# Performance work log

Hardware: AMD Instinct MI355X
Metric: run time of the kernel (lower is better)

The kernel has to match this reference:

```python
import jax, jax.numpy as jnp
import numpy as np

NUM_GROUPS = 32
EPS = 1e-6


def group_norm(x, scale, bias):
    # x: [B, C, H, W]
    b, c, h, w = x.shape
    g = NUM_GROUPS
    xg = x.reshape(b, g, c // g, h, w)
    mean = xg.mean(axis=(2, 3, 4), keepdims=True)
    var = xg.var(axis=(2, 3, 4), keepdims=True)
    xg = (xg - mean) * jax.lax.rsqrt(var + EPS)
    x = xg.reshape(b, c, h, w)
    return x * scale[None, :, None, None] + bias[None, :, None, None]


def conv1x1(x, w, b):
    # x: [B, C, H, W], w: [O, C] (1x1 conv weight), b: [O]
    return jnp.einsum('oc,bchw->bohw', w, x) + b[None, :, None, None]


def setup_inputs() -> dict:
    key = jax.random.key(0)
    ks = jax.random.split(key, 6)
    B, C, H, W = 8, 512, 64, 64
    s = 1.0 / np.sqrt(C)
    return {
        'x': jax.random.normal(ks[0], (B, C, H, W), dtype=jnp.float32),
        'gn_scale': jnp.ones((C,), jnp.float32),
        'gn_bias': jnp.zeros((C,), jnp.float32),
        'wq': jax.random.normal(ks[1], (C, C), jnp.float32) * s,
        'bq': jnp.zeros((C,), jnp.float32),
        'wk': jax.random.normal(ks[2], (C, C), jnp.float32) * s,
        'bk': jnp.zeros((C,), jnp.float32),
        'wv': jax.random.normal(ks[3], (C, C), jnp.float32) * s,
        'bv': jnp.zeros((C,), jnp.float32),
        'wo': jax.random.normal(ks[4], (C, C), jnp.float32) * s,
        'bo': jnp.zeros((C,), jnp.float32),
    }


def reference(x, gn_scale, gn_bias, wq, bq, wk, bk, wv, bv, wo, bo):
    b, c, h, w = x.shape
    h_ = group_norm(x, gn_scale, gn_bias)
    q = conv1x1(h_, wq, bq).reshape(b, c, h * w)  # [B, C, N]
    k = conv1x1(h_, wk, bk).reshape(b, c, h * w)
    v = conv1x1(h_, wv, bv).reshape(b, c, h * w)
    scale = c ** (-0.5)
    # scores[b, i, j] = sum_c q[b,c,i] * k[b,c,j]
    scores = jnp.einsum('bci,bcj->bij', q, k) * scale
    attn = jax.nn.softmax(scores, axis=2)  # softmax over key positions j
    # h_[b, c, i] = sum_j v[b,c,j] * attn[b,i,j]
    out = jnp.einsum('bcj,bij->bci', v, attn).reshape(b, c, h, w)
    out = conv1x1(out, wo, bo)
    return x + out
```

## Files before the change

kernel.cpp:

```cpp
#include <hip/hip_runtime.h>

using u16 = unsigned short;
using s16x8 = __attribute__((ext_vector_type(8))) short;
using f32x4 = __attribute__((ext_vector_type(4))) float;
using f32x16 = __attribute__((ext_vector_type(16))) float;

#define DEV static __device__ __forceinline__

DEV u16 bf16b(float f) {
  unsigned u = __builtin_bit_cast(unsigned, f);
  return (u16)((u + 0x7fffu + ((u >> 16) & 1u)) >> 16);
}

DEV void gload16(const void* g, void* l) {
  __builtin_amdgcn_global_load_lds((const __attribute__((address_space(1))) unsigned int*)g,
                                   (__attribute__((address_space(3))) unsigned int*)l, 16, 0, 0);
}

DEV f32x4 mfma16(s16x8 a, s16x8 b, f32x4 c) {
  return __builtin_amdgcn_mfma_f32_16x16x32_bf16(a, b, c, 0, 0, 0);
}
DEV f32x16 mfma32(s16x8 a, s16x8 b, f32x16 c) {
  return __builtin_amdgcn_mfma_f32_32x32x16_bf16(a, b, c, 0, 0, 0);
}

__global__ void k_cvt_w(const float* __restrict__ w0, const float* __restrict__ w1,
                        const float* __restrict__ w2, const float* __restrict__ w3,
                        u16* __restrict__ out) {
  int i = blockIdx.x * 256 + threadIdx.x;
  int which = i >> 18, off = i & 0x3ffff;
  const float* s = which == 0 ? w0 : which == 1 ? w1 : which == 2 ? w2 : w3;
  out[i] = bf16b(s[off]);
}

__global__ __launch_bounds__(1024) void k_gn(const float* __restrict__ x,
                                             const float* __restrict__ gsc,
                                             const float* __restrict__ gbi,
                                             u16* __restrict__ hT) {
  const int b = blockIdx.x >> 5, g = blockIdx.x & 31;
  const int tid = threadIdx.x;
  const float* xs = x + (size_t)(b * 512 + g * 16) * 4096;

  float s = 0.f, s2 = 0.f;
  const float4* xv = (const float4*)xs;
  #pragma unroll
  for (int kq = 0; kq < 16; kq++) {
    float4 v = xv[tid + kq * 1024];
    s  += v.x + v.y + v.z + v.w;
    s2 += v.x * v.x + v.y * v.y + v.z * v.z + v.w * v.w;
  }
  #pragma unroll
  for (int m = 1; m < 64; m <<= 1) { s += __shfl_xor(s, m, 64); s2 += __shfl_xor(s2, m, 64); }
  __shared__ float rs[16], rs2[16];
  __shared__ float stat[2];
  int wid = tid >> 6;
  if ((tid & 63) == 0) { rs[wid] = s; rs2[wid] = s2; }
  __syncthreads();
  if (tid == 0) {
    float a = 0.f, a2 = 0.f;
    for (int i = 0; i < 16; i++) { a += rs[i]; a2 += rs2[i]; }
    float mean = a * (1.f / 65536.f);
    float var = a2 * (1.f / 65536.f) - mean * mean;
    stat[0] = mean;
    stat[1] = rsqrtf(var + 1e-6f);
  }
  __syncthreads();
  const float mean = stat[0], rstd = stat[1];
  const int cc = tid & 15;
  const float aa = rstd * gsc[g * 16 + cc];
  const float bb = gbi[g * 16 + cc] - mean * aa;

  __shared__ float tile[16][257];
  u16* ho = hT + (size_t)b * 4096 * 512 + g * 16;
  for (int n0 = 0; n0 < 4096; n0 += 256) {
    __syncthreads();
    #pragma unroll
    for (int rr = 0; rr < 4; rr++) {
      int r = rr * 4 + (tid >> 8);
      tile[r][tid & 255] = xs[(size_t)r * 4096 + n0 + (tid & 255)];
    }
    __syncthreads();
    #pragma unroll
    for (int kq = 0; kq < 4; kq++) {
      int nl = ((tid >> 4) << 2) + kq;
      float v = tile[cc][nl];
      ho[(size_t)(n0 + nl) * 512 + cc] = bf16b(v * aa + bb);
    }
  }
}

template<bool BIAS_ROW, bool RESID>
DEV void gemm_nt_core(const u16* __restrict__ A, const u16* __restrict__ Bm,
                      const float* __restrict__ bias, const float* __restrict__ resid,
                      void* __restrict__ outp, int m0, int n0, int ldo) {
  __shared__ __align__(16) u16 As[128 * 64];
  __shared__ __align__(16) u16 Bs[128 * 64];
  const int tid = threadIdx.x;
  const int lane = tid & 63;
  const int w = tid >> 6;
  const int wr = w >> 1, wc = w & 1;
  f32x4 acc[4][4] = {};

  for (int kc = 0; kc < 8; kc++) {
    #pragma unroll
    for (int q = 0; q < 4; q++) {
      int idx = q * 256 + tid;
      int row = idx >> 3, sl = idx & 7;
      int koff = kc * 64 + ((sl ^ (row & 7)) << 3);
      gload16(A  + (size_t)(m0 + row) * 512 + koff, As + (q * 256 + w * 64) * 8);
      gload16(Bm + (size_t)(n0 + row) * 512 + koff, Bs + (q * 256 + w * 64) * 8);
    }
    __syncthreads();
    #pragma unroll
    for (int kk = 0; kk < 2; kk++) {
      s16x8 af[4], bfr[4];
      #pragma unroll
      for (int m = 0; m < 4; m++) {
        int row = wr * 64 + m * 16 + (lane & 15);
        int cq = kk * 4 + (lane >> 4);
        af[m] = *(const s16x8*)&As[row * 64 + ((cq ^ (row & 7)) << 3)];
      }
      #pragma unroll
      for (int n = 0; n < 4; n++) {
        int row = wc * 64 + n * 16 + (lane & 15);
        int cq = kk * 4 + (lane >> 4);
        bfr[n] = *(const s16x8*)&Bs[row * 64 + ((cq ^ (row & 7)) << 3)];
      }
      #pragma unroll
      for (int m = 0; m < 4; m++)
        #pragma unroll
        for (int n = 0; n < 4; n++)
          acc[m][n] = mfma16(af[m], bfr[n], acc[m][n]);
    }
    __syncthreads();
  }

  float bcol[4];
  if (!BIAS_ROW) {
    #pragma unroll
    for (int n = 0; n < 4; n++) bcol[n] = bias[n0 + wc * 64 + n * 16 + (lane & 15)];
  }
  #pragma unroll
  for (int m = 0; m < 4; m++) {
    #pragma unroll
    for (int r = 0; r < 4; r++) {
      int row = m0 + wr * 64 + m * 16 + ((lane >> 4) << 2) + r;
      float badd = BIAS_ROW ? bias[row] : 0.f;
      #pragma unroll
      for (int n = 0; n < 4; n++) {
        int col = n0 + wc * 64 + n * 16 + (lane & 15);
        float v = acc[m][n][r] + (BIAS_ROW ? badd : bcol[n]);
        if (RESID) {
          size_t o = (size_t)row * ldo + col;
          ((float*)outp)[o] = v + resid[o];
        } else {
          ((u16*)outp)[(size_t)row * ldo + col] = bf16b(v);
        }
      }
    }
  }
}

__global__ __launch_bounds__(256) void k_gemm_qk(const u16* __restrict__ hT,
    const u16* __restrict__ wqb, const u16* __restrict__ wkb,
    const float* __restrict__ bq, const float* __restrict__ bk,
    u16* __restrict__ qT, u16* __restrict__ kT) {
  int z = blockIdx.z, b = z >> 1;
  const u16* A = hT + (size_t)b * 4096 * 512;
  const u16* W = (z & 1) ? wkb : wqb;
  const float* bb = (z & 1) ? bk : bq;
  u16* out = ((z & 1) ? kT : qT) + (size_t)b * 4096 * 512;
  gemm_nt_core<false, false>(A, W, bb, nullptr, out, blockIdx.x * 128, blockIdx.y * 128, 512);
}

__global__ __launch_bounds__(256) void k_gemm_v(const u16* __restrict__ wvb,
    const u16* __restrict__ hT, const float* __restrict__ bv, u16* __restrict__ vS) {
  int b = blockIdx.z;
  gemm_nt_core<true, false>(wvb, hT + (size_t)b * 4096 * 512, bv, nullptr,
                            vS + (size_t)b * 512 * 4096, blockIdx.x * 128, blockIdx.y * 128, 4096);
}

__global__ __launch_bounds__(256) void k_gemm_o(const u16* __restrict__ wob,
    const u16* __restrict__ oT, const float* __restrict__ bo,
    const float* __restrict__ x, float* __restrict__ y) {
  int b = blockIdx.z;
  gemm_nt_core<true, true>(wob, oT + (size_t)b * 4096 * 512, bo,
                           x + (size_t)b * 512 * 4096,
                           y + (size_t)b * 512 * 4096, blockIdx.x * 128, blockIdx.y * 128, 4096);
}

__global__ __launch_bounds__(512) void k_attn(const u16* __restrict__ qT,
                                              const u16* __restrict__ kT,
                                              const u16* __restrict__ vS,
                                              u16* __restrict__ oT) {
  const int it = blockIdx.x, b = blockIdx.y;
  const int tid = threadIdx.x, lane = tid & 63, w = tid >> 6;
  const int rg = w >> 1, cg = w & 1;
  const int rg2 = w >> 2, cg2 = w & 3;

  const u16* qp = qT + (size_t)b * 4096 * 512;
  const u16* kp = kT + (size_t)b * 4096 * 512;
  const u16* vp = vS + (size_t)b * 512 * 4096;

  __shared__ __align__(16) u16 Ks[2][32 * 512];
  __shared__ __align__(16) u16 Vs[2][512 * 32];
  __shared__ __align__(16) u16 Ps[64 * 32];
  __shared__ float l_lds[2][64];

  s16x8 qf[16];
  {
    const u16* qrow = qp + (size_t)(it * 64 + rg * 16 + (lane & 15)) * 512 + ((lane >> 4) << 3);
    #pragma unroll
    for (int t = 0; t < 16; t++) qf[t] = *(const s16x8*)(qrow + t * 32);
  }
  f32x16 oacc[4] = {};
  float lpart[4] = {0.f, 0.f, 0.f, 0.f};

  const int wbase = w * 64 * 8;

  #pragma unroll
  for (int q = 0; q < 4; q++) {
    int d = q * 512 + tid, j = d >> 6, p = d & 63;
    gload16(kp + (size_t)j * 512 + ((p ^ (j & 7)) << 3), Ks[0] + q * 4096 + wbase);
  }
  #pragma unroll
  for (int q = 0; q < 4; q++) {
    int d = q * 512 + tid, c = d >> 2, p = d & 3;
    gload16(vp + (size_t)c * 4096 + ((p ^ ((c >> 1) & 3)) << 3), Vs[0] + q * 4096 + wbase);
  }
  __syncthreads();

  const float se = 0.044194173824159216f;
  const int jS = cg * 16 + (lane & 15);
  const int xmS = (jS & 7) << 3;
  const int irow = rg2 * 32 + (lane & 31);
  const int sband = lane >> 5;

  for (int jt = 0; jt < 128; jt++) {
    const int cur = jt & 1, nxt = cur ^ 1;
    if (jt < 127) {
      const u16* kn = kp + (size_t)(jt + 1) * 32 * 512;
      #pragma unroll
      for (int q = 0; q < 4; q++) {
        int d = q * 512 + tid, j = d >> 6, p = d & 63;
        gload16(kn + (size_t)j * 512 + ((p ^ (j & 7)) << 3), Ks[nxt] + q * 4096 + wbase);
      }
    }
    {
      f32x4 sacc = {};
      const u16* kb = Ks[cur] + jS * 512;
      #pragma unroll
      for (int t = 0; t < 16; t++) {
        int off = (((t * 4 + (lane >> 4)) << 3)) ^ xmS;
        sacc = mfma16(qf[t], *(const s16x8*)(kb + off), sacc);
      }
      #pragma unroll
      for (int r = 0; r < 4; r++) {
        float pv = __expf(sacc[r] * se);
        lpart[r] += pv;
        int grow = rg * 16 + ((lane >> 4) << 2) + r;
        int psl = ((jS >> 3) ^ ((grow >> 1) & 3)) & 3;
        Ps[grow * 32 + psl * 8 + (jS & 7)] = bf16b(pv);
      }
    }
    __syncthreads();

    if (jt < 127) {
      const u16* vn = vp + (size_t)(jt + 1) * 32;
      #pragma unroll
      for (int q = 0; q < 4; q++) {
        int d = q * 512 + tid, c = d >> 2, p = d & 3;
        gload16(vn + (size_t)c * 4096 + ((p ^ ((c >> 1) & 3)) << 3), Vs[nxt] + q * 4096 + wbase);
      }
    }
    #pragma unroll
    for (int ks = 0; ks < 2; ks++) {
      int s = ks * 2 + sband;
      int pp = (s ^ ((irow >> 1) & 3)) & 3;
      s16x8 pf = *(const s16x8*)(Ps + irow * 32 + pp * 8);
      #pragma unroll
      for (int n = 0; n < 4; n++) {
        int c = cg2 * 128 + n * 32 + (lane & 31);
        int vpp = (s ^ ((c >> 1) & 3)) & 3;
        s16x8 vf = *(const s16x8*)(Vs[cur] + c * 32 + vpp * 8);
        oacc[n] = mfma32(pf, vf, oacc[n]);
      }
    }
    __syncthreads();
  }

  #pragma unroll
  for (int r = 0; r < 4; r++) {
    float lv = lpart[r];
    lv += __shfl_xor(lv, 1, 64);
    lv += __shfl_xor(lv, 2, 64);
    lv += __shfl_xor(lv, 4, 64);
    lv += __shfl_xor(lv, 8, 64);
    if ((lane & 15) == 0) l_lds[cg][rg * 16 + ((lane >> 4) << 2) + r] = lv;
  }
  __syncthreads();

  float linv[16];
  #pragma unroll
  for (int e = 0; e < 16; e++) {
    int i = rg2 * 32 + (e & 3) + 8 * (e >> 2) + 4 * sband;
    linv[e] = 1.0f / (l_lds[0][i] + l_lds[1][i]);
  }
  u16* op = oT + ((size_t)b * 4096 + it * 64) * 512;
  #pragma unroll
  for (int n = 0; n < 4; n++) {
    int col = cg2 * 128 + n * 32 + (lane & 31);
    #pragma unroll
    for (int e = 0; e < 16; e++) {
      int i = rg2 * 32 + (e & 3) + 8 * (e >> 2) + 4 * sband;
      op[(size_t)i * 512 + col] = bf16b(oacc[n][e] * linv[e]);
    }
  }
}

extern "C" void kernel_launch(void* const* d_in, const int* in_sizes, int n_in,
                              void* d_out, int out_size, void* d_ws, size_t ws_size,
                              hipStream_t stream) {
  const float* x   = (const float*)d_in[0];
  const float* gsc = (const float*)d_in[1];
  const float* gbi = (const float*)d_in[2];
  const float* wq  = (const float*)d_in[3];
  const float* bq  = (const float*)d_in[4];
  const float* wk  = (const float*)d_in[5];
  const float* bk  = (const float*)d_in[6];
  const float* wv  = (const float*)d_in[7];
  const float* bv  = (const float*)d_in[8];
  const float* wo  = (const float*)d_in[9];
  const float* bo  = (const float*)d_in[10];
  float* out = (float*)d_out;
  char* ws = (char*)d_ws;

  u16* hT = (u16*)ws;
  u16* vS = (u16*)(ws + ((size_t)32 << 20));
  u16* wB = (u16*)(ws + ((size_t)64 << 20));
  u16* wqb = wB;
  u16* wkb = wB + 262144;
  u16* wvb = wB + 2 * 262144;
  u16* wob = wB + 3 * 262144;
  u16* qT = (u16*)d_out;
  u16* kT = qT + (size_t)8 * 4096 * 512;

  k_cvt_w<<<4096, 256, 0, stream>>>(wq, wk, wv, wo, wB);
  k_gn<<<256, 1024, 0, stream>>>(x, gsc, gbi, hT);
  k_gemm_qk<<<dim3(32, 4, 16), 256, 0, stream>>>(hT, wqb, wkb, bq, bk, qT, kT);
  k_gemm_v<<<dim3(4, 32, 8), 256, 0, stream>>>(wvb, hT, bv, vS);
  k_attn<<<dim3(64, 8), 512, 0, stream>>>(qT, kT, vS, hT );
  k_gemm_o<<<dim3(4, 32, 8), 256, 0, stream>>>(wob, hT, bo, x, out);
}
```

Measured before the change: 754.6 us.

## Software-pipeline attention P·V with register V loads and double-buffer GEMM LDS

The attention kernel drops the V tile from LDS and loads V fragments straight from global memory into registers. P is double-buffered so each iteration's P·V MFMAs use the previous tile's probabilities, leaving one barrier per key tile instead of two. The QK^T chain is split across four independent accumulators to shorten the MFMA dependency chain. The projection GEMM gets double-buffered LDS so the next K-chunk loads while the current one computes. The trade-off is more registers for V fragments and uncached strided global loads of V.

```diff
diff --git a/kernel.cpp b/kernel.cpp
--- a/kernel.cpp
+++ b/kernel.cpp
@@ -93,24 +93,33 @@
 DEV void gemm_nt_core(const u16* __restrict__ A, const u16* __restrict__ Bm,
                       const float* __restrict__ bias, const float* __restrict__ resid,
                       void* __restrict__ outp, int m0, int n0, int ldo) {
-  __shared__ __align__(16) u16 As[128 * 64];
-  __shared__ __align__(16) u16 Bs[128 * 64];
+  __shared__ __align__(16) u16 As[2][128 * 64];
+  __shared__ __align__(16) u16 Bs[2][128 * 64];
   const int tid = threadIdx.x;
   const int lane = tid & 63;
   const int w = tid >> 6;
   const int wr = w >> 1, wc = w & 1;
   f32x4 acc[4][4] = {};
 
+  #define STAGE_G(kc, buf)                                                    \
+    {                                                                         \
+      int koffb = (kc) * 64;                                                  \
+      _Pragma("unroll")                                                       \
+      for (int q = 0; q < 4; q++) {                                           \
+        int idx = q * 256 + tid;                                              \
+        int row = idx >> 3, sl = idx & 7;                                     \
+        int koff = koffb + ((sl ^ (row & 7)) << 3);                           \
+        gload16(A  + (size_t)(m0 + row) * 512 + koff, As[buf] + (q * 256 + w * 64) * 8); \
+        gload16(Bm + (size_t)(n0 + row) * 512 + koff, Bs[buf] + (q * 256 + w * 64) * 8); \
+      }                                                                       \
+    }
+
+  STAGE_G(0, 0);
+  __syncthreads();
+
   for (int kc = 0; kc < 8; kc++) {
-    #pragma unroll
-    for (int q = 0; q < 4; q++) {
-      int idx = q * 256 + tid;
-      int row = idx >> 3, sl = idx & 7;
-      int koff = kc * 64 + ((sl ^ (row & 7)) << 3);
-      gload16(A  + (size_t)(m0 + row) * 512 + koff, As + (q * 256 + w * 64) * 8);
-      gload16(Bm + (size_t)(n0 + row) * 512 + koff, Bs + (q * 256 + w * 64) * 8);
-    }
-    __syncthreads();
+    const int cur = kc & 1;
+    if (kc < 7) STAGE_G(kc + 1, cur ^ 1);
     #pragma unroll
     for (int kk = 0; kk < 2; kk++) {
       s16x8 af[4], bfr[4];
@@ -118,13 +127,13 @@
       for (int m = 0; m < 4; m++) {
         int row = wr * 64 + m * 16 + (lane & 15);
         int cq = kk * 4 + (lane >> 4);
-        af[m] = *(const s16x8*)&As[row * 64 + ((cq ^ (row & 7)) << 3)];
+        af[m] = *(const s16x8*)&As[cur][row * 64 + ((cq ^ (row & 7)) << 3)];
       }
       #pragma unroll
       for (int n = 0; n < 4; n++) {
         int row = wc * 64 + n * 16 + (lane & 15);
         int cq = kk * 4 + (lane >> 4);
-        bfr[n] = *(const s16x8*)&Bs[row * 64 + ((cq ^ (row & 7)) << 3)];
+        bfr[n] = *(const s16x8*)&Bs[cur][row * 64 + ((cq ^ (row & 7)) << 3)];
       }
       #pragma unroll
       for (int m = 0; m < 4; m++)
@@ -134,6 +143,7 @@
     }
     __syncthreads();
   }
+  #undef STAGE_G
 
   float bcol[4];
   if (!BIAS_ROW) {
@@ -203,8 +213,7 @@
   const u16* vp = vS + (size_t)b * 512 * 4096;
 
   __shared__ __align__(16) u16 Ks[2][32 * 512];
-  __shared__ __align__(16) u16 Vs[2][512 * 32];
-  __shared__ __align__(16) u16 Ps[64 * 32];
+  __shared__ __align__(16) u16 Ps[2][64 * 32];
   __shared__ float l_lds[2][64];
 
   s16x8 qf[16];
@@ -215,78 +224,82 @@
   }
   f32x16 oacc[4] = {};
   float lpart[4] = {0.f, 0.f, 0.f, 0.f};
+  s16x8 vf[2][4];
 
   const int wbase = w * 64 * 8;
+  const int sb = lane >> 5;
+  const int jS = cg * 16 + (lane & 15);
+  const int irow = rg2 * 32 + (lane & 31);
+  const u16* vbase = vp + (size_t)(cg2 * 128 + (lane & 31)) * 4096 + sb * 8;
 
   #pragma unroll
   for (int q = 0; q < 4; q++) {
     int d = q * 512 + tid, j = d >> 6, p = d & 63;
     gload16(kp + (size_t)j * 512 + ((p ^ (j & 7)) << 3), Ks[0] + q * 4096 + wbase);
   }
-  #pragma unroll
-  for (int q = 0; q < 4; q++) {
-    int d = q * 512 + tid, c = d >> 2, p = d & 3;
-    gload16(vp + (size_t)c * 4096 + ((p ^ ((c >> 1) & 3)) << 3), Vs[0] + q * 4096 + wbase);
-  }
   __syncthreads();
 
   const float se = 0.044194173824159216f;
-  const int jS = cg * 16 + (lane & 15);
-  const int xmS = (jS & 7) << 3;
-  const int irow = rg2 * 32 + (lane & 31);
-  const int sband = lane >> 5;
 
   for (int jt = 0; jt < 128; jt++) {
-    const int cur = jt & 1, nxt = cur ^ 1;
+    const int cur = jt & 1;
+
+    if (jt > 0) {
+      const u16* pr = Ps[cur ^ 1] + irow * 32;
+      #pragma unroll
+      for (int ks = 0; ks < 2; ks++) {
+        int q = ks * 2 + sb;
+        s16x8 pf = *(const s16x8*)(pr + ((q ^ (irow & 3)) << 3));
+        #pragma unroll
+        for (int n = 0; n < 4; n++) oacc[n] = mfma32(pf, vf[ks][n], oacc[n]);
+      }
+    }
+    {
+      const u16* vj = vbase + jt * 32;
+      #pragma unroll
+      for (int ks = 0; ks < 2; ks++)
+        #pragma unroll
+        for (int n = 0; n < 4; n++)
+          vf[ks][n] = *(const s16x8*)(vj + (size_t)n * 32 * 4096 + ks * 16);
+    }
     if (jt < 127) {
       const u16* kn = kp + (size_t)(jt + 1) * 32 * 512;
       #pragma unroll
       for (int q = 0; q < 4; q++) {
         int d = q * 512 + tid, j = d >> 6, p = d & 63;
-        gload16(kn + (size_t)j * 512 + ((p ^ (j & 7)) << 3), Ks[nxt] + q * 4096 + wbase);
+        gload16(kn + (size_t)j * 512 + ((p ^ (j & 7)) << 3), Ks[cur ^ 1] + q * 4096 + wbase);
       }
     }
     {
-      f32x4 sacc = {};
+      f32x4 sc[4] = {{}, {}, {}, {}};
       const u16* kb = Ks[cur] + jS * 512;
+      const int xm = (jS & 7) << 3;
       #pragma unroll
       for (int t = 0; t < 16; t++) {
-        int off = (((t * 4 + (lane >> 4)) << 3)) ^ xmS;
-        sacc = mfma16(qf[t], *(const s16x8*)(kb + off), sacc);
-      }
+        int off = ((t * 4 + (lane >> 4)) << 3) ^ xm;
+        sc[t & 3] = mfma16(qf[t], *(const s16x8*)(kb + off), sc[t & 3]);
+      }
+      f32x4 sm = (sc[0] + sc[1]) + (sc[2] + sc[3]);
       #pragma unroll
       for (int r = 0; r < 4; r++) {
-        float pv = __expf(sacc[r] * se);
+        float pv = __expf(sm[r] * se);
         lpart[r] += pv;
         int grow = rg * 16 + ((lane >> 4) << 2) + r;
-        int psl = ((jS >> 3) ^ ((grow >> 1) & 3)) & 3;
-        Ps[grow * 32 + psl * 8 + (jS & 7)] = bf16b(pv);
+        Ps[cur][grow * 32 + (((jS >> 3) ^ (grow & 3)) << 3) + (jS & 7)] = bf16b(pv);
       }
     }
     __syncthreads();
-
-    if (jt < 127) {
-      const u16* vn = vp + (size_t)(jt + 1) * 32;
-      #pragma unroll
-      for (int q = 0; q < 4; q++) {
-        int d = q * 512 + tid, c = d >> 2, p = d & 3;
-        gload16(vn + (size_t)c * 4096 + ((p ^ ((c >> 1) & 3)) << 3), Vs[nxt] + q * 4096 + wbase);
-      }
-    }
+  }
+
+  {
+    const u16* pr = Ps[1] + irow * 32;
     #pragma unroll
     for (int ks = 0; ks < 2; ks++) {
-      int s = ks * 2 + sband;
-      int pp = (s ^ ((irow >> 1) & 3)) & 3;
-      s16x8 pf = *(const s16x8*)(Ps + irow * 32 + pp * 8);
-      #pragma unroll
-      for (int n = 0; n < 4; n++) {
-        int c = cg2 * 128 + n * 32 + (lane & 31);
-        int vpp = (s ^ ((c >> 1) & 3)) & 3;
-        s16x8 vf = *(const s16x8*)(Vs[cur] + c * 32 + vpp * 8);
-        oacc[n] = mfma32(pf, vf, oacc[n]);
-      }
-    }
-    __syncthreads();
+      int q = ks * 2 + sb;
+      s16x8 pf = *(const s16x8*)(pr + ((q ^ (irow & 3)) << 3));
+      #pragma unroll
+      for (int n = 0; n < 4; n++) oacc[n] = mfma32(pf, vf[ks][n], oacc[n]);
+    }
   }
 
   #pragma unroll
@@ -303,7 +316,7 @@
   float linv[16];
   #pragma unroll
   for (int e = 0; e < 16; e++) {
-    int i = rg2 * 32 + (e & 3) + 8 * (e >> 2) + 4 * sband;
+    int i = rg2 * 32 + (e & 3) + 8 * (e >> 2) + 4 * sb;
     linv[e] = 1.0f / (l_lds[0][i] + l_lds[1][i]);
   }
   u16* op = oT + ((size_t)b * 4096 + it * 64) * 512;
@@ -312,7 +325,7 @@
     int col = cg2 * 128 + n * 32 + (lane & 31);
     #pragma unroll
     for (int e = 0; e < 16; e++) {
-      int i = rg2 * 32 + (e & 3) + 8 * (e >> 2) + 4 * sband;
+      int i = rg2 * 32 + (e & 3) + 8 * (e >> 2) + 4 * sb;
       op[(size_t)i * 512 + col] = bf16b(oacc[n][e] * linv[e]);
     }
   }
```

Result: slower. 1.060 ms (+40.5%).
